# Kernel optimization log

Hardware: AMD Instinct MI355X
Metric: run time of the kernel (lower is better)

The kernel has to match this reference:

```python
import jax, jax.numpy as jnp
import numpy as np

USER_NUM = 50000
ITEM_NUM = 100000
N = USER_NUM + ITEM_NUM
D = 64
NUM_LAYERS = 3          # len(hidden_units) in config
MAIN_LAYERS = NUM_LAYERS + 1  # forward() loops over hidden_units AFTER prepending embedding_dim
LMBD = 1e-4
SSL_TAU = 0.5
SSL_WEIGHT = 0.1
E = 2_000_000
E_KEEP = 1_800_000
EPS = 1e-12


def _edge_weights(src, dst, n):
    # calculate_graph: norm = out_degree^-0.5, edge_weight = norm[src]*norm[dst]
    deg = jnp.zeros((n,), jnp.float32).at[src].add(1.0)
    norm = jnp.power(jnp.maximum(deg, 1.0), -0.5)
    return norm[src] * norm[dst]


def setup_inputs() -> dict:
    key = jax.random.key(0)
    ks = jax.random.split(key, 12)
    user_emb = jax.random.normal(ks[0], (USER_NUM, D), jnp.float32) * 0.1
    item_emb = jax.random.normal(ks[1], (ITEM_NUM, D), jnp.float32) * 0.1
    src = jax.random.randint(ks[2], (E,), 0, N)
    dst = jax.random.randint(ks[3], (E,), 0, N)
    w = _edge_weights(src, dst, N)
    # augmented graphs (ED): random edge subset + self loops
    self_loop = jnp.arange(N, dtype=src.dtype)
    src1 = jnp.concatenate([jax.random.randint(ks[4], (E_KEEP - N,), 0, N) if E_KEEP - N > 0 else src[:0], jax.random.randint(ks[4], (E_KEEP - N,), 0, N)[:0], self_loop])
    src1 = jnp.concatenate([jax.random.randint(ks[4], (E_KEEP,), 0, N), self_loop])
    dst1 = jnp.concatenate([jax.random.randint(ks[5], (E_KEEP,), 0, N), self_loop])
    src1 = src1[: E_KEEP + N - 0]
    w1 = _edge_weights(src1, dst1, N)
    src2 = jnp.concatenate([jax.random.randint(ks[6], (E_KEEP,), 0, N), self_loop])
    dst2 = jnp.concatenate([jax.random.randint(ks[7], (E_KEEP,), 0, N), self_loop])
    w2 = _edge_weights(src2, dst2, N)
    user_id = jax.random.randint(ks[8], (4096,), 0, USER_NUM)
    item_id = jax.random.randint(ks[9], (4096,), 0, ITEM_NUM)
    neg_item_id = jax.random.randint(ks[10], (4096,), 0, ITEM_NUM)
    return {"user_emb": user_emb, "item_emb": item_emb, "src": src, "dst": dst, "w": w,
            "src1": src1, "dst1": dst1, "w1": w1, "src2": src2, "dst2": dst2, "w2": w2,
            "user_id": user_id, "item_id": item_id, "neg_item_id": neg_item_id}


def _l2norm(x):
    n = jnp.linalg.norm(x, axis=1, keepdims=True)
    return x / jnp.maximum(n, EPS)


def _propagate(user_emb, item_emb, src, dst, w, layers):
    # LightGCNConv per layer: m = h[src]*w; h' = scatter-sum to dst; L2 normalize
    u_list, i_list = [user_emb], [item_emb]
    u, i = user_emb, item_emb
    for _ in range(layers):
        h = jnp.concatenate([u, i], axis=0)            # [N, D]
        m = h[src] * w[:, None]                        # [E, D]
        h = jax.ops.segment_sum(m, dst, num_segments=N)
        h = _l2norm(h)
        u, i = h[:USER_NUM], h[USER_NUM:]
        u_list.append(u)
        i_list.append(i)
    fu = jnp.mean(jnp.stack(u_list, axis=1), axis=1)
    fi = jnp.mean(jnp.stack(i_list, axis=1), axis=1)
    return fu, fi


def reference(user_emb, item_emb, src, dst, w, src1, dst1, w1, src2, dst2, w2, user_id, item_id, neg_item_id):
    # main propagation (note: MAIN_LAYERS = NUM_LAYERS+1, faithful to the source bug)
    fu, fi = _propagate(user_emb, item_emb, src, dst, w, MAIN_LAYERS)
    ue = fu[user_id]
    pe = fi[item_id]
    ne = fi[neg_item_id]
    # BPR loss
    pos = jnp.sum(ue * pe, axis=1)
    neg = jnp.sum(ue * ne, axis=1)
    bpr = -jnp.mean(jax.nn.log_sigmoid(pos - neg))
    reg = (jnp.sum(ue ** 2) + jnp.sum(pe ** 2) + jnp.sum(ne ** 2)) / 2.0
    bpr_loss = bpr + LMBD * reg / ue.shape[0]
    # SSL loss on two augmented views (NUM_LAYERS layers each)
    u1, i1 = _propagate(user_emb, item_emb, src1, dst1, w1, NUM_LAYERS)
    u2, i2 = _propagate(user_emb, item_emb, src2, dst2, w2, NUM_LAYERS)
    ue1 = _l2norm(u1[user_id]); ue2 = _l2norm(u2[user_id]); au2 = _l2norm(u2)
    v1 = jnp.exp(jnp.sum(ue1 * ue2, axis=1) / SSL_TAU)
    v2 = jnp.sum(jnp.exp(ue1 @ au2.T / SSL_TAU), axis=1)
    ssl_user = -jnp.sum(jnp.log(v1 / v2))
    ie1 = _l2norm(i1[item_id]); ie2 = _l2norm(i2[item_id]); ai2 = _l2norm(i2)
    v3 = jnp.exp(jnp.sum(ie1 * ie2, axis=1) / SSL_TAU)
    v4 = jnp.sum(jnp.exp(ie1 @ ai2.T / SSL_TAU), axis=1)
    ssl_item = -jnp.sum(jnp.log(v3 / v4))
    ssl_loss = (ssl_item + ssl_user) * SSL_WEIGHT
    return bpr_loss + ssl_loss
```

## Files before the change

kernel.cpp:

```cpp
#include <hip/hip_runtime.h>
#include <math.h>
#include <stdint.h>

#define USER_NUM 50000
#define ITEM_NUM 100000
#define NN (USER_NUM + ITEM_NUM)
#define D 64
#define TAU_INV 2.0f
#define LMBD 0.0001f
#define NCITER 16
#define NRG 64
#define T3 (3 * NN)
#define NBLK3 ((T3 + 255) / 256)

typedef __bf16 bf16x8 __attribute__((ext_vector_type(8)));
typedef float  f32x4  __attribute__((ext_vector_type(4)));

static __device__ __forceinline__ unsigned short f2bf(float x) {
    union { float f; unsigned u; } v; v.f = x;
    unsigned r = v.u + 0x7FFFu + ((v.u >> 16) & 1u);
    return (unsigned short)(r >> 16);
}
static __device__ __forceinline__ float bf2f(unsigned short b) {
    union { unsigned u; float f; } v; v.u = ((unsigned)b) << 16;
    return v.f;
}

__global__ void init_kernel(const float* __restrict__ ue, const float* __restrict__ ie,
                            unsigned short* __restrict__ hb, float* __restrict__ acc) {
    int i = blockIdx.x * 256 + threadIdx.x;
    if (i < NN * D) {
        float v = (i < USER_NUM * D) ? ue[i] : ie[i - USER_NUM * D];
        hb[i] = f2bf(v); acc[i] = v;
    }
}

__global__ void deg3_kernel(const int* __restrict__ d0, const int* __restrict__ d1,
                            const int* __restrict__ d2, int* __restrict__ deg3,
                            int E0, int E1, int E2) {
    int i = blockIdx.x * 256 + threadIdx.x;
    int d;
    if (i < E0) d = d0[i];
    else if (i < E0 + E1) d = NN + d1[i - E0];
    else if (i < E0 + E1 + E2) d = 2 * NN + d2[i - E0 - E1];
    else return;
    atomicAdd(&deg3[d], 1);
}

__global__ void scan_reduce_kernel(const int* __restrict__ deg, int* __restrict__ bsum) {
    __shared__ int sd[256];
    int tid = threadIdx.x;
    int i = blockIdx.x * 256 + tid;
    sd[tid] = (i < T3) ? deg[i] : 0;
    __syncthreads();
    for (int o = 128; o; o >>= 1) { if (tid < o) sd[tid] += sd[tid + o]; __syncthreads(); }
    if (tid == 0) bsum[blockIdx.x] = sd[0];
}

__global__ void scan_mid_kernel(int* __restrict__ bsum, int* __restrict__ totp, int nblk) {
    __shared__ int sd[1024];
    int tid = threadIdx.x;
    int v0 = (2 * tid < nblk) ? bsum[2 * tid] : 0;
    int v1 = (2 * tid + 1 < nblk) ? bsum[2 * tid + 1] : 0;
    sd[tid] = v0 + v1;
    __syncthreads();
    for (int o = 1; o < 1024; o <<= 1) {
        int t = (tid >= o) ? sd[tid - o] : 0;
        __syncthreads();
        sd[tid] += t;
        __syncthreads();
    }
    int base = tid ? sd[tid - 1] : 0;
    if (2 * tid < nblk) bsum[2 * tid] = base;
    if (2 * tid + 1 < nblk) bsum[2 * tid + 1] = base + v0;
    if (tid == 1023) totp[0] = sd[1023];
}

__global__ void scan_final_kernel(const int* __restrict__ deg, const int* __restrict__ bsum,
                                  int* __restrict__ rowptr, int* __restrict__ cursor) {
    __shared__ int sd[256];
    int tid = threadIdx.x;
    int i = blockIdx.x * 256 + tid;
    int v = (i < T3) ? deg[i] : 0;
    sd[tid] = v;
    __syncthreads();
    for (int o = 1; o < 256; o <<= 1) {
        int t = (tid >= o) ? sd[tid - o] : 0;
        __syncthreads();
        sd[tid] += t;
        __syncthreads();
    }
    if (i < T3) {
        int ex = sd[tid] - v + bsum[blockIdx.x];
        rowptr[i] = ex;
        cursor[i] = ex;
    }
}

__global__ void fill3_kernel(const int* __restrict__ s0, const int* __restrict__ d0, const float* __restrict__ w0,
                             const int* __restrict__ s1, const int* __restrict__ d1, const float* __restrict__ w1,
                             const int* __restrict__ s2, const int* __restrict__ d2, const float* __restrict__ w2,
                             int* __restrict__ cursor, int2* __restrict__ perm,
                             int E0, int E1, int E2) {
    int i = blockIdx.x * 256 + threadIdx.x;
    int d, s; float w;
    if (i < E0) { d = d0[i]; s = s0[i]; w = w0[i]; }
    else if (i < E0 + E1) { int j = i - E0; d = NN + d1[j]; s = s1[j]; w = w1[j]; }
    else if (i < E0 + E1 + E2) { int j = i - E0 - E1; d = 2 * NN + d2[j]; s = s2[j]; w = w2[j]; }
    else return;
    int p = atomicAdd(&cursor[d], 1);
    perm[p] = make_int2(s, __float_as_int(w));
}

__global__ __launch_bounds__(256) void gather_norm_kernel(const unsigned short* __restrict__ hb,
        const int* __restrict__ rowptr, const int2* __restrict__ perm,
        unsigned short* __restrict__ hn, float* __restrict__ acc) {
    int gid = blockIdx.x * 256 + threadIdx.x;
    int row = gid >> 6;
    int lane = gid & 63;
    if (row >= NN) return;
    int beg = rowptr[row];
    int end = rowptr[row + 1];
    float s = 0.f;
    int e = beg;
    for (; e + 4 <= end; e += 4) {
        int2 p0 = perm[e];
        int2 p1 = perm[e + 1];
        int2 p2 = perm[e + 2];
        int2 p3 = perm[e + 3];
        float v0 = bf2f(hb[(size_t)p0.x * D + lane]);
        float v1 = bf2f(hb[(size_t)p1.x * D + lane]);
        float v2 = bf2f(hb[(size_t)p2.x * D + lane]);
        float v3 = bf2f(hb[(size_t)p3.x * D + lane]);
        s += v0 * __int_as_float(p0.y) + v1 * __int_as_float(p1.y)
           + v2 * __int_as_float(p2.y) + v3 * __int_as_float(p3.y);
    }
    for (; e < end; e++) {
        int2 p0 = perm[e];
        s += bf2f(hb[(size_t)p0.x * D + lane]) * __int_as_float(p0.y);
    }
    float q = s * s;
    #pragma unroll
    for (int o = 32; o; o >>= 1) q += __shfl_xor(q, o);
    float y = s / fmaxf(sqrtf(q), 1e-12f);
    size_t idx = (size_t)row * D + lane;
    hn[idx] = f2bf(y);
    acc[idx] += y;
}

__global__ void norm_rows_bf_kernel(float* __restrict__ h, unsigned short* __restrict__ hb) {
    int gid = blockIdx.x * 256 + threadIdx.x;
    int row = gid >> 6;
    int lane = gid & 63;
    if (row >= NN) return;
    size_t idx = (size_t)row * D + lane;
    float x = h[idx];
    float s = x * x;
    #pragma unroll
    for (int o = 32; o; o >>= 1) s += __shfl_xor(s, o);
    float y = x / fmaxf(sqrtf(s), 1e-12f);
    h[idx] = y;
    hb[idx] = f2bf(y);
}

__global__ void bpr_kernel(const float* __restrict__ acc, const int* __restrict__ uid,
                           const int* __restrict__ iid, const int* __restrict__ nid,
                           float* __restrict__ scal, int B) {
    int gid = blockIdx.x * 256 + threadIdx.x;
    int r = gid >> 6;
    int lane = gid & 63;
    if (r >= B) return;
    const float inv = 1.0f / 5.0f;
    float ue = acc[(size_t)uid[r] * D + lane] * inv;
    float pe = acc[(size_t)(USER_NUM + iid[r]) * D + lane] * inv;
    float ne = acc[(size_t)(USER_NUM + nid[r]) * D + lane] * inv;
    float pos = ue * pe, neg = ue * ne, reg = ue * ue + pe * pe + ne * ne;
    #pragma unroll
    for (int o = 32; o; o >>= 1) {
        pos += __shfl_xor(pos, o);
        neg += __shfl_xor(neg, o);
        reg += __shfl_xor(reg, o);
    }
    if (lane == 0) {
        float x = pos - neg;
        float ls = (x >= 0.f) ? (-log1pf(expf(-x))) : (x - log1pf(expf(x)));
        atomicAdd(&scal[0], -ls);
        atomicAdd(&scal[1], reg * 0.5f);
    }
}

__global__ void extract_norm_kernel(const float* __restrict__ acc, const int* __restrict__ uid,
                                    const int* __restrict__ iid, unsigned short* __restrict__ ue1b,
                                    unsigned short* __restrict__ ie1b, int B) {
    int gid = blockIdx.x * 256 + threadIdx.x;
    int t = gid >> 6;
    int lane = gid & 63;
    if (t >= 2 * B) return;
    bool user = (t < B);
    int r = user ? t : (t - B);
    size_t srow = user ? (size_t)uid[r] * D : (size_t)(USER_NUM + iid[r]) * D;
    float x = acc[srow + lane];
    float s = x * x;
    #pragma unroll
    for (int o = 32; o; o >>= 1) s += __shfl_xor(s, o);
    float y = x / fmaxf(sqrtf(s), 1e-12f);
    (user ? ue1b : ie1b)[(size_t)r * D + lane] = f2bf(y);
}

__global__ __launch_bounds__(256) void ssl_mfma_kernel(const unsigned short* __restrict__ Ab,
                                                       const unsigned short* __restrict__ Bb,
                                                       float* __restrict__ rowsum,
                                                       int M, int nc) {
    int bid = blockIdx.x;
    int xcd = bid & 7;
    int inner = bid >> 3;
    int rg = inner & (NRG - 1);
    int cgrp = inner >> 6;
    int colChunk = cgrp * 8 + xcd;
    if (colChunk >= nc) return;

    int wave = threadIdx.x >> 6;
    int lane = threadIdx.x & 63;
    int l15 = lane & 15;
    int lg  = lane >> 4;
    int rgbase = rg * 64;
    int chunkbase = colChunk * (128 * NCITER);

    bf16x8 afr[4][2];
    {
        const unsigned short* ab = Ab + (size_t)(rgbase + l15) * D + lg * 8;
        #pragma unroll
        for (int i = 0; i < 4; i++) {
            afr[i][0] = *(const bf16x8*)(ab + (size_t)i * 16 * D);
            afr[i][1] = *(const bf16x8*)(ab + (size_t)i * 16 * D + 32);
        }
    }

    float rowacc[4][4];
    #pragma unroll
    for (int i = 0; i < 4; i++)
        #pragma unroll
        for (int r = 0; r < 4; r++) rowacc[i][r] = 0.f;

    for (int it = 0; it < NCITER; it++) {
        int cb = chunkbase + it * 128 + wave * 32;
        bf16x8 bfr[2][2];
        bool val[2];
        #pragma unroll
        for (int cf = 0; cf < 2; cf++) {
            int col = cb + cf * 16 + l15;
            val[cf] = (col < M);
            int cc = val[cf] ? col : (M - 1);
            const unsigned short* bp = Bb + (size_t)cc * D + lg * 8;
            bfr[cf][0] = *(const bf16x8*)(bp);
            bfr[cf][1] = *(const bf16x8*)(bp + 32);
        }

        f32x4 acc[4][2];
        #pragma unroll
        for (int i = 0; i < 4; i++)
            #pragma unroll
            for (int cf = 0; cf < 2; cf++)
                acc[i][cf] = (f32x4){0.f, 0.f, 0.f, 0.f};

        #pragma unroll
        for (int i = 0; i < 4; i++) {
            #pragma unroll
            for (int cf = 0; cf < 2; cf++) {
                acc[i][cf] = __builtin_amdgcn_mfma_f32_16x16x32_bf16(afr[i][0], bfr[cf][0], acc[i][cf], 0, 0, 0);
                acc[i][cf] = __builtin_amdgcn_mfma_f32_16x16x32_bf16(afr[i][1], bfr[cf][1], acc[i][cf], 0, 0, 0);
            }
        }

        #pragma unroll
        for (int i = 0; i < 4; i++) {
            #pragma unroll
            for (int r = 0; r < 4; r++) {
                float e0 = val[0] ? __expf(TAU_INV * acc[i][0][r]) : 0.f;
                float e1 = val[1] ? __expf(TAU_INV * acc[i][1][r]) : 0.f;
                rowacc[i][r] += e0 + e1;
            }
        }
    }

    #pragma unroll
    for (int i = 0; i < 4; i++) {
        #pragma unroll
        for (int r = 0; r < 4; r++) {
            float s = rowacc[i][r];
            s += __shfl_xor(s, 1);
            s += __shfl_xor(s, 2);
            s += __shfl_xor(s, 4);
            s += __shfl_xor(s, 8);
            if (l15 == 0) atomicAdd(&rowsum[rgbase + i * 16 + lg * 4 + r], s);
        }
    }
}

__global__ void ssl_fin_kernel(const unsigned short* __restrict__ ue1b,
                               const unsigned short* __restrict__ ie1b,
                               const float* __restrict__ A2, const int* __restrict__ uid,
                               const int* __restrict__ iid, const float* __restrict__ rsU,
                               const float* __restrict__ rsI, float* __restrict__ scal, int B) {
    int gid = blockIdx.x * 256 + threadIdx.x;
    int t = gid >> 6;
    int lane = gid & 63;
    if (t >= 2 * B) return;
    bool user = (t < B);
    int r = user ? t : (t - B);
    const unsigned short* a = (user ? ue1b : ie1b) + (size_t)r * D;
    size_t brow = user ? (size_t)uid[r] * D : (size_t)(USER_NUM + iid[r]) * D;
    float p = bf2f(a[lane]) * A2[brow + lane];
    #pragma unroll
    for (int o = 32; o; o >>= 1) p += __shfl_xor(p, o);
    if (lane == 0) {
        float contrib = logf((user ? rsU : rsI)[r]) - p * TAU_INV;
        atomicAdd(&scal[user ? 2 : 3], contrib);
    }
}

__global__ void final_kernel(const float* __restrict__ scal, float* __restrict__ out, int B) {
    if (threadIdx.x == 0 && blockIdx.x == 0) {
        float invB = 1.0f / (float)B;
        float bpr_loss = scal[0] * invB + LMBD * scal[1] * invB;
        float ssl_loss = (scal[2] + scal[3]) * 0.1f;
        out[0] = bpr_loss + ssl_loss;
    }
}

extern "C" void kernel_launch(void* const* d_in, const int* in_sizes, int n_in,
                              void* d_out, int out_size, void* d_ws, size_t ws_size,
                              hipStream_t stream) {
    const float* user_emb = (const float*)d_in[0];
    const float* item_emb = (const float*)d_in[1];
    const int*   src  = (const int*)d_in[2];
    const int*   dst  = (const int*)d_in[3];
    const float* w    = (const float*)d_in[4];
    const int*   src1 = (const int*)d_in[5];
    const int*   dst1 = (const int*)d_in[6];
    const float* w1   = (const float*)d_in[7];
    const int*   src2 = (const int*)d_in[8];
    const int*   dst2 = (const int*)d_in[9];
    const float* w2   = (const float*)d_in[10];
    const int* user_id = (const int*)d_in[11];
    const int* item_id = (const int*)d_in[12];
    const int* neg_id  = (const int*)d_in[13];
    int E0 = in_sizes[2];
    int E1 = in_sizes[5];
    int E2 = in_sizes[8];
    int B  = in_sizes[11];
    int ET = E0 + E1 + E2;

    size_t nd = (size_t)NN * D;
    float* acc = (float*)d_ws;
    unsigned short* hAb = (unsigned short*)(acc + nd);
    unsigned short* hBb = hAb + nd;
    unsigned short* ue1b = hBb + nd;
    unsigned short* ie1b = ue1b + (size_t)B * D;
    float* rsU  = (float*)(ie1b + (size_t)B * D);
    float* rsI  = rsU + B;
    float* scal = rsI + B;
    int* deg3    = (int*)(scal + 8);
    int* rowptr3 = deg3 + T3;
    int* cursor3 = rowptr3 + T3 + 1;
    int* bsum3   = cursor3 + T3;
    int2* perm3  = (int2*)(((uintptr_t)(bsum3 + 2048) + 15) & ~(uintptr_t)15);
    unsigned short* bbuf = hAb;

    hipMemsetAsync(rsU, 0, (size_t)(2 * B + 8) * sizeof(float), stream);
    hipMemsetAsync(deg3, 0, (size_t)T3 * sizeof(int), stream);

    int gridElem = (NN * D + 255) / 256;
    int gridRows = (NN * 64 + 255) / 256;
    int gridE3 = (ET + 255) / 256;

    deg3_kernel<<<gridE3, 256, 0, stream>>>(dst, dst1, dst2, deg3, E0, E1, E2);
    scan_reduce_kernel<<<NBLK3, 256, 0, stream>>>(deg3, bsum3);
    scan_mid_kernel<<<1, 1024, 0, stream>>>(bsum3, rowptr3 + T3, NBLK3);
    scan_final_kernel<<<NBLK3, 256, 0, stream>>>(deg3, bsum3, rowptr3, cursor3);
    fill3_kernel<<<gridE3, 256, 0, stream>>>(src, dst, w, src1, dst1, w1, src2, dst2, w2,
                                             cursor3, perm3, E0, E1, E2);

    auto propagate = [&](int g, int layers) {
        const int* rp = rowptr3 + (size_t)g * NN;
        init_kernel<<<gridElem, 256, 0, stream>>>(user_emb, item_emb, hAb, acc);
        unsigned short* cur = hAb;
        unsigned short* nxt = hBb;
        for (int l = 0; l < layers; l++) {
            gather_norm_kernel<<<gridRows, 256, 0, stream>>>(cur, rp, perm3, nxt, acc);
            unsigned short* t = cur; cur = nxt; nxt = t;
        }
    };

    propagate(0, 4);
    bpr_kernel<<<(B * 64) / 256, 256, 0, stream>>>(acc, user_id, item_id, neg_id, scal, B);

    propagate(1, 3);
    extract_norm_kernel<<<(2 * B * 64) / 256, 256, 0, stream>>>(acc, user_id, item_id, ue1b, ie1b, B);

    propagate(2, 3);
    norm_rows_bf_kernel<<<gridRows, 256, 0, stream>>>(acc, bbuf);

    {
        int ncU = (USER_NUM + 128 * NCITER - 1) / (128 * NCITER);
        int gu = 8 * NRG * ((ncU + 7) / 8);
        ssl_mfma_kernel<<<gu, 256, 0, stream>>>(ue1b, bbuf, rsU, USER_NUM, ncU);
        int ncI = (ITEM_NUM + 128 * NCITER - 1) / (128 * NCITER);
        int gi = 8 * NRG * ((ncI + 7) / 8);
        ssl_mfma_kernel<<<gi, 256, 0, stream>>>(ie1b, bbuf + (size_t)USER_NUM * D, rsI, ITEM_NUM, ncI);
    }

    ssl_fin_kernel<<<(2 * B * 64) / 256, 256, 0, stream>>>(ue1b, ie1b, acc, user_id, item_id,
                                                           rsU, rsI, scal, B);
    final_kernel<<<1, 64, 0, stream>>>(scal, (float*)d_out, B);
}
```

Baseline: 2.045 ms.

## Store per-layer bf16 outputs instead of fp32 accumulator; partition CSR build by XCD

Removes the fp32 accumulator that every gather layer read and wrote. Each layer's bf16 output now goes to its own buffer, and the layer sum is rebuilt only where it is needed: the BPR rows, the extracted SSL rows, and one final sum-and-normalize pass. The embedding init now runs once instead of once per propagation. Degree counting and CSR fill are split by blockIdx&7 so that each group of blocks handles only destinations in one eighth of the range, which aims to keep atomics local to an XCD. The cost is that every edge is read eight times, and the layer sums lose some precision because they are built from bf16 values rather than accumulated in fp32.

```diff
diff --git a/kernel.cpp b/kernel.cpp
--- a/kernel.cpp
+++ b/kernel.cpp
@@ -12,6 +12,8 @@
 #define NRG 64
 #define T3 (3 * NN)
 #define NBLK3 ((T3 + 255) / 256)
+#define EPB 8192
+#define RR (T3 / 8)
 
 typedef __bf16 bf16x8 __attribute__((ext_vector_type(8)));
 typedef float  f32x4  __attribute__((ext_vector_type(4)));
@@ -27,24 +29,30 @@
 }
 
 __global__ void init_kernel(const float* __restrict__ ue, const float* __restrict__ ie,
-                            unsigned short* __restrict__ hb, float* __restrict__ acc) {
+                            unsigned short* __restrict__ h0) {
     int i = blockIdx.x * 256 + threadIdx.x;
     if (i < NN * D) {
         float v = (i < USER_NUM * D) ? ue[i] : ie[i - USER_NUM * D];
-        hb[i] = f2bf(v); acc[i] = v;
-    }
-}
-
-__global__ void deg3_kernel(const int* __restrict__ d0, const int* __restrict__ d1,
-                            const int* __restrict__ d2, int* __restrict__ deg3,
-                            int E0, int E1, int E2) {
-    int i = blockIdx.x * 256 + threadIdx.x;
-    int d;
-    if (i < E0) d = d0[i];
-    else if (i < E0 + E1) d = NN + d1[i - E0];
-    else if (i < E0 + E1 + E2) d = 2 * NN + d2[i - E0 - E1];
-    else return;
-    atomicAdd(&deg3[d], 1);
+        h0[i] = f2bf(v);
+    }
+}
+
+__global__ __launch_bounds__(256) void deg3p_kernel(const int* __restrict__ d0,
+        const int* __restrict__ d1, const int* __restrict__ d2,
+        int* __restrict__ degD3, int E0, int E1, int E2, int ET) {
+    int xcd = blockIdx.x & 7;
+    int chunk = blockIdx.x >> 3;
+    int base = chunk * EPB;
+    int lo = xcd * RR, hi = lo + RR;
+    for (int k = threadIdx.x; k < EPB; k += 256) {
+        int i = base + k;
+        if (i >= ET) break;
+        int g;
+        if (i < E0) g = d0[i];
+        else if (i < E0 + E1) g = NN + d1[i - E0];
+        else g = 2 * NN + d2[i - E0 - E1];
+        if (g >= lo && g < hi) atomicAdd(&degD3[g], 1);
+    }
 }
 
 __global__ void scan_reduce_kernel(const int* __restrict__ deg, int* __restrict__ bsum) {
@@ -97,24 +105,43 @@
     }
 }
 
-__global__ void fill3_kernel(const int* __restrict__ s0, const int* __restrict__ d0, const float* __restrict__ w0,
-                             const int* __restrict__ s1, const int* __restrict__ d1, const float* __restrict__ w1,
-                             const int* __restrict__ s2, const int* __restrict__ d2, const float* __restrict__ w2,
-                             int* __restrict__ cursor, int2* __restrict__ perm,
-                             int E0, int E1, int E2) {
-    int i = blockIdx.x * 256 + threadIdx.x;
-    int d, s; float w;
-    if (i < E0) { d = d0[i]; s = s0[i]; w = w0[i]; }
-    else if (i < E0 + E1) { int j = i - E0; d = NN + d1[j]; s = s1[j]; w = w1[j]; }
-    else if (i < E0 + E1 + E2) { int j = i - E0 - E1; d = 2 * NN + d2[j]; s = s2[j]; w = w2[j]; }
-    else return;
-    int p = atomicAdd(&cursor[d], 1);
-    perm[p] = make_int2(s, __float_as_int(w));
-}
-
-__global__ __launch_bounds__(256) void gather_norm_kernel(const unsigned short* __restrict__ hb,
+__global__ __launch_bounds__(256) void fill3p_kernel(
+        const int* __restrict__ s0, const int* __restrict__ d0, const float* __restrict__ w0,
+        const int* __restrict__ s1, const int* __restrict__ d1, const float* __restrict__ w1,
+        const int* __restrict__ s2, const int* __restrict__ d2, const float* __restrict__ w2,
+        int* __restrict__ cursor, int2* __restrict__ perm,
+        int E0, int E1, int E2, int ET) {
+    int xcd = blockIdx.x & 7;
+    int chunk = blockIdx.x >> 3;
+    int base = chunk * EPB;
+    int lo = xcd * RR, hi = lo + RR;
+    for (int k = threadIdx.x; k < EPB; k += 256) {
+        int i = base + k;
+        if (i >= ET) break;
+        int g, s; float w;
+        if (i < E0) {
+            g = d0[i];
+            if (g < lo || g >= hi) continue;
+            s = s0[i]; w = w0[i];
+        } else if (i < E0 + E1) {
+            int j = i - E0;
+            g = NN + d1[j];
+            if (g < lo || g >= hi) continue;
+            s = s1[j]; w = w1[j];
+        } else {
+            int j = i - E0 - E1;
+            g = 2 * NN + d2[j];
+            if (g < lo || g >= hi) continue;
+            s = s2[j]; w = w2[j];
+        }
+        int p = atomicAdd(&cursor[g], 1);
+        perm[p] = make_int2(s, __float_as_int(w));
+    }
+}
+
+__global__ __launch_bounds__(256) void gather_kernel(const unsigned short* __restrict__ hb,
         const int* __restrict__ rowptr, const int2* __restrict__ perm,
-        unsigned short* __restrict__ hn, float* __restrict__ acc) {
+        unsigned short* __restrict__ hn) {
     int gid = blockIdx.x * 256 + threadIdx.x;
     int row = gid >> 6;
     int lane = gid & 63;
@@ -143,37 +170,30 @@
     #pragma unroll
     for (int o = 32; o; o >>= 1) q += __shfl_xor(q, o);
     float y = s / fmaxf(sqrtf(q), 1e-12f);
-    size_t idx = (size_t)row * D + lane;
-    hn[idx] = f2bf(y);
-    acc[idx] += y;
-}
-
-__global__ void norm_rows_bf_kernel(float* __restrict__ h, unsigned short* __restrict__ hb) {
-    int gid = blockIdx.x * 256 + threadIdx.x;
-    int row = gid >> 6;
-    int lane = gid & 63;
-    if (row >= NN) return;
-    size_t idx = (size_t)row * D + lane;
-    float x = h[idx];
-    float s = x * x;
-    #pragma unroll
-    for (int o = 32; o; o >>= 1) s += __shfl_xor(s, o);
-    float y = x / fmaxf(sqrtf(s), 1e-12f);
-    h[idx] = y;
-    hb[idx] = f2bf(y);
-}
-
-__global__ void bpr_kernel(const float* __restrict__ acc, const int* __restrict__ uid,
-                           const int* __restrict__ iid, const int* __restrict__ nid,
-                           float* __restrict__ scal, int B) {
+    hn[(size_t)row * D + lane] = f2bf(y);
+}
+
+static __device__ __forceinline__ float emb_at(const float* ue, const float* ie,
+                                               int grow, int lane) {
+    return (grow < USER_NUM) ? ue[(size_t)grow * D + lane]
+                             : ie[(size_t)(grow - USER_NUM) * D + lane];
+}
+
+__global__ void bpr_kernel(const float* __restrict__ ue_, const float* __restrict__ ie_,
+                           const unsigned short* __restrict__ h1, const unsigned short* __restrict__ h2,
+                           const unsigned short* __restrict__ h3, const unsigned short* __restrict__ h4,
+                           const int* __restrict__ uid, const int* __restrict__ iid,
+                           const int* __restrict__ nid, float* __restrict__ scal, int B) {
     int gid = blockIdx.x * 256 + threadIdx.x;
     int r = gid >> 6;
     int lane = gid & 63;
     if (r >= B) return;
-    const float inv = 1.0f / 5.0f;
-    float ue = acc[(size_t)uid[r] * D + lane] * inv;
-    float pe = acc[(size_t)(USER_NUM + iid[r]) * D + lane] * inv;
-    float ne = acc[(size_t)(USER_NUM + nid[r]) * D + lane] * inv;
+    int g0 = uid[r], g1 = USER_NUM + iid[r], g2 = USER_NUM + nid[r];
+    size_t i0 = (size_t)g0 * D + lane, i1 = (size_t)g1 * D + lane, i2 = (size_t)g2 * D + lane;
+    const float inv = 0.2f;
+    float ue = (emb_at(ue_, ie_, g0, lane) + bf2f(h1[i0]) + bf2f(h2[i0]) + bf2f(h3[i0]) + bf2f(h4[i0])) * inv;
+    float pe = (emb_at(ue_, ie_, g1, lane) + bf2f(h1[i1]) + bf2f(h2[i1]) + bf2f(h3[i1]) + bf2f(h4[i1])) * inv;
+    float ne = (emb_at(ue_, ie_, g2, lane) + bf2f(h1[i2]) + bf2f(h2[i2]) + bf2f(h3[i2]) + bf2f(h4[i2])) * inv;
     float pos = ue * pe, neg = ue * ne, reg = ue * ue + pe * pe + ne * ne;
     #pragma unroll
     for (int o = 32; o; o >>= 1) {
@@ -189,8 +209,12 @@
     }
 }
 
-__global__ void extract_norm_kernel(const float* __restrict__ acc, const int* __restrict__ uid,
-                                    const int* __restrict__ iid, unsigned short* __restrict__ ue1b,
+__global__ void extract_norm_kernel(const float* __restrict__ ue_, const float* __restrict__ ie_,
+                                    const unsigned short* __restrict__ h1,
+                                    const unsigned short* __restrict__ h2,
+                                    const unsigned short* __restrict__ h3,
+                                    const int* __restrict__ uid, const int* __restrict__ iid,
+                                    unsigned short* __restrict__ ue1b,
                                     unsigned short* __restrict__ ie1b, int B) {
     int gid = blockIdx.x * 256 + threadIdx.x;
     int t = gid >> 6;
@@ -198,13 +222,31 @@
     if (t >= 2 * B) return;
     bool user = (t < B);
     int r = user ? t : (t - B);
-    size_t srow = user ? (size_t)uid[r] * D : (size_t)(USER_NUM + iid[r]) * D;
-    float x = acc[srow + lane];
+    int grow = user ? uid[r] : (USER_NUM + iid[r]);
+    size_t idx = (size_t)grow * D + lane;
+    float x = emb_at(ue_, ie_, grow, lane) + bf2f(h1[idx]) + bf2f(h2[idx]) + bf2f(h3[idx]);
     float s = x * x;
     #pragma unroll
     for (int o = 32; o; o >>= 1) s += __shfl_xor(s, o);
     float y = x / fmaxf(sqrtf(s), 1e-12f);
     (user ? ue1b : ie1b)[(size_t)r * D + lane] = f2bf(y);
+}
+
+__global__ void sum_norm_all_kernel(const float* __restrict__ ue_, const float* __restrict__ ie_,
+                                    const unsigned short* __restrict__ h1,
+                                    const unsigned short* __restrict__ h2,
+                                    const unsigned short* __restrict__ h3,
+                                    unsigned short* __restrict__ out) {
+    int gid = blockIdx.x * 256 + threadIdx.x;
+    int row = gid >> 6;
+    int lane = gid & 63;
+    if (row >= NN) return;
+    size_t idx = (size_t)row * D + lane;
+    float x = emb_at(ue_, ie_, row, lane) + bf2f(h1[idx]) + bf2f(h2[idx]) + bf2f(h3[idx]);
+    float s = x * x;
+    #pragma unroll
+    for (int o = 32; o; o >>= 1) s += __shfl_xor(s, o);
+    out[idx] = f2bf(x / fmaxf(sqrtf(s), 1e-12f));
 }
 
 __global__ __launch_bounds__(256) void ssl_mfma_kernel(const unsigned short* __restrict__ Ab,
@@ -299,9 +341,10 @@
 
 __global__ void ssl_fin_kernel(const unsigned short* __restrict__ ue1b,
                                const unsigned short* __restrict__ ie1b,
-                               const float* __restrict__ A2, const int* __restrict__ uid,
-                               const int* __restrict__ iid, const float* __restrict__ rsU,
-                               const float* __restrict__ rsI, float* __restrict__ scal, int B) {
+                               const unsigned short* __restrict__ A2b,
+                               const int* __restrict__ uid, const int* __restrict__ iid,
+                               const float* __restrict__ rsU, const float* __restrict__ rsI,
+                               float* __restrict__ scal, int B) {
     int gid = blockIdx.x * 256 + threadIdx.x;
     int t = gid >> 6;
     int lane = gid & 63;
@@ -310,7 +353,7 @@
     int r = user ? t : (t - B);
     const unsigned short* a = (user ? ue1b : ie1b) + (size_t)r * D;
     size_t brow = user ? (size_t)uid[r] * D : (size_t)(USER_NUM + iid[r]) * D;
-    float p = bf2f(a[lane]) * A2[brow + lane];
+    float p = bf2f(a[lane]) * bf2f(A2b[brow + lane]);
     #pragma unroll
     for (int o = 32; o; o >>= 1) p += __shfl_xor(p, o);
     if (lane == 0) {
@@ -352,65 +395,67 @@
     int ET = E0 + E1 + E2;
 
     size_t nd = (size_t)NN * D;
-    float* acc = (float*)d_ws;
-    unsigned short* hAb = (unsigned short*)(acc + nd);
-    unsigned short* hBb = hAb + nd;
-    unsigned short* ue1b = hBb + nd;
+    unsigned short* h0 = (unsigned short*)d_ws;
+    unsigned short* h1 = h0 + nd;
+    unsigned short* h2 = h1 + nd;
+    unsigned short* h3 = h2 + nd;
+    unsigned short* h4 = h3 + nd;
+    unsigned short* ue1b = h4 + nd;
     unsigned short* ie1b = ue1b + (size_t)B * D;
     float* rsU  = (float*)(ie1b + (size_t)B * D);
     float* rsI  = rsU + B;
     float* scal = rsI + B;
-    int* deg3    = (int*)(scal + 8);
-    int* rowptr3 = deg3 + T3;
+    int* degD3   = (int*)(scal + 8);
+    int* rowptr3 = degD3 + T3;
     int* cursor3 = rowptr3 + T3 + 1;
     int* bsum3   = cursor3 + T3;
     int2* perm3  = (int2*)(((uintptr_t)(bsum3 + 2048) + 15) & ~(uintptr_t)15);
-    unsigned short* bbuf = hAb;
 
     hipMemsetAsync(rsU, 0, (size_t)(2 * B + 8) * sizeof(float), stream);
-    hipMemsetAsync(deg3, 0, (size_t)T3 * sizeof(int), stream);
+    hipMemsetAsync(degD3, 0, (size_t)T3 * sizeof(int), stream);
 
     int gridElem = (NN * D + 255) / 256;
     int gridRows = (NN * 64 + 255) / 256;
-    int gridE3 = (ET + 255) / 256;
-
-    deg3_kernel<<<gridE3, 256, 0, stream>>>(dst, dst1, dst2, deg3, E0, E1, E2);
-    scan_reduce_kernel<<<NBLK3, 256, 0, stream>>>(deg3, bsum3);
+    int gridE8 = 8 * ((ET + EPB - 1) / EPB);
+
+    init_kernel<<<gridElem, 256, 0, stream>>>(user_emb, item_emb, h0);
+
+    deg3p_kernel<<<gridE8, 256, 0, stream>>>(dst, dst1, dst2, degD3, E0, E1, E2, ET);
+    scan_reduce_kernel<<<NBLK3, 256, 0, stream>>>(degD3, bsum3);
     scan_mid_kernel<<<1, 1024, 0, stream>>>(bsum3, rowptr3 + T3, NBLK3);
-    scan_final_kernel<<<NBLK3, 256, 0, stream>>>(deg3, bsum3, rowptr3, cursor3);
-    fill3_kernel<<<gridE3, 256, 0, stream>>>(src, dst, w, src1, dst1, w1, src2, dst2, w2,
-                                             cursor3, perm3, E0, E1, E2);
-
+    scan_final_kernel<<<NBLK3, 256, 0, stream>>>(degD3, bsum3, rowptr3, cursor3);
+    fill3p_kernel<<<gridE8, 256, 0, stream>>>(src, dst, w, src1, dst1, w1, src2, dst2, w2,
+                                              cursor3, perm3, E0, E1, E2, ET);
+
+    unsigned short* hs[5] = {h0, h1, h2, h3, h4};
     auto propagate = [&](int g, int layers) {
         const int* rp = rowptr3 + (size_t)g * NN;
-        init_kernel<<<gridElem, 256, 0, stream>>>(user_emb, item_emb, hAb, acc);
-        unsigned short* cur = hAb;
-        unsigned short* nxt = hBb;
-        for (int l = 0; l < layers; l++) {
-            gather_norm_kernel<<<gridRows, 256, 0, stream>>>(cur, rp, perm3, nxt, acc);
-            unsigned short* t = cur; cur = nxt; nxt = t;
+        for (int l = 1; l <= layers; l++) {
+            gather_kernel<<<gridRows, 256, 0, stream>>>(hs[l - 1], rp, perm3, hs[l]);
         }
     };
 
     propagate(0, 4);
-    bpr_kernel<<<(B * 64) / 256, 256, 0, stream>>>(acc, user_id, item_id, neg_id, scal, B);
+    bpr_kernel<<<(B * 64) / 256, 256, 0, stream>>>(user_emb, item_emb, h1, h2, h3, h4,
+                                                   user_id, item_id, neg_id, scal, B);
 
     propagate(1, 3);
-    extract_norm_kernel<<<(2 * B * 64) / 256, 256, 0, stream>>>(acc, user_id, item_id, ue1b, ie1b, B);
+    extract_norm_kernel<<<(2 * B * 64) / 256, 256, 0, stream>>>(user_emb, item_emb, h1, h2, h3,
+                                                                user_id, item_id, ue1b, ie1b, B);
 
     propagate(2, 3);
-    norm_rows_bf_kernel<<<gridRows, 256, 0, stream>>>(acc, bbuf);
+    sum_norm_all_kernel<<<gridRows, 256, 0, stream>>>(user_emb, item_emb, h1, h2, h3, h4);
 
     {
         int ncU = (USER_NUM + 128 * NCITER - 1) / (128 * NCITER);
         int gu = 8 * NRG * ((ncU + 7) / 8);
-        ssl_mfma_kernel<<<gu, 256, 0, stream>>>(ue1b, bbuf, rsU, USER_NUM, ncU);
+        ssl_mfma_kernel<<<gu, 256, 0, stream>>>(ue1b, h4, rsU, USER_NUM, ncU);
         int ncI = (ITEM_NUM + 128 * NCITER - 1) / (128 * NCITER);
         int gi = 8 * NRG * ((ncI + 7) / 8);
-        ssl_mfma_kernel<<<gi, 256, 0, stream>>>(ie1b, bbuf + (size_t)USER_NUM * D, rsI, ITEM_NUM, ncI);
-    }
-
-    ssl_fin_kernel<<<(2 * B * 64) / 256, 256, 0, stream>>>(ue1b, ie1b, acc, user_id, item_id,
+        ssl_mfma_kernel<<<gi, 256, 0, stream>>>(ie1b, h4 + (size_t)USER_NUM * D, rsI, ITEM_NUM, ncI);
+    }
+
+    ssl_fin_kernel<<<(2 * B * 64) / 256, 256, 0, stream>>>(ue1b, ie1b, h4, user_id, item_id,
                                                            rsU, rsI, scal, B);
     final_kernel<<<1, 64, 0, stream>>>(scal, (float*)d_out, B);
 }
```

Measured after the change: 2.000 ms. 2.2% less time.
